# Performance work log

Measured on AMD Instinct MI355X. Metric: run time of the kernel, lower is better.

The kernel has to match this reference:

```python
import jax, jax.numpy as jnp
import numpy as np

D_MODEL = 1024
SEL_DIM = 64
CONFIGS = [(4, 32), (8, 64), (16, 128)]  # (heads, dim)
B, T = 2, 2048


def setup_inputs() -> dict:
    key = jax.random.key(0)
    ks = jax.random.split(key, 20)
    s = 0.02  # init scale for stability
    inp = {
        "x": jax.random.normal(ks[0], (B, T, D_MODEL), jnp.float32),
        "sel_w1": jax.random.normal(ks[1], (SEL_DIM, D_MODEL), jnp.float32) * s,
        "sel_b1": jnp.zeros((SEL_DIM,), jnp.float32),
        "sel_w2": jax.random.normal(ks[2], (SEL_DIM, SEL_DIM), jnp.float32) * s,
        "sel_b2": jnp.zeros((SEL_DIM,), jnp.float32),
        "sel_w3": jax.random.normal(ks[3], (len(CONFIGS), SEL_DIM), jnp.float32) * s,
        "sel_b3": jnp.zeros((len(CONFIGS),), jnp.float32),
    }
    for i, (h, d) in enumerate(CONFIGS):
        inp[f"qw{i}"] = jax.random.normal(ks[4 + 3 * i], (h * d, D_MODEL), jnp.float32) * s
        inp[f"kw{i}"] = jax.random.normal(ks[5 + 3 * i], (d, D_MODEL), jnp.float32) * s
        inp[f"ww{i}"] = jax.random.normal(ks[6 + 3 * i], (h, D_MODEL), jnp.float32) * s
    return inp


def _seq_features(x):
    # x: [b,t,d]
    b, t, d = x.shape
    seq_mean = jnp.mean(x, axis=1, keepdims=True)            # [b,1,d]
    seq_std = jnp.std(x, axis=1, keepdims=True, ddof=1)      # torch.std is unbiased
    pos = (jnp.arange(t, dtype=x.dtype) / t)[None, :, None]  # [1,t,1] broadcast to [b,t,d]
    return x + seq_mean + seq_std + pos * 0.1


def _forward(x, sel_w1, sel_b1, sel_w2, sel_b2, sel_w3, sel_b3,
             qw0, kw0, ww0, qw1, kw1, ww1, qw2, kw2, ww2):
    b, t, dm = x.shape
    feats = _seq_features(x)
    h1 = jax.nn.relu(feats @ sel_w1.T + sel_b1)
    h2 = jax.nn.relu(h1 @ sel_w2.T + sel_b2)
    config_probs = jax.nn.softmax(h2 @ sel_w3.T + sel_b3, axis=-1)  # [b,t,ncfg]

    per_cfg = [(qw0, kw0, ww0), (qw1, kw1, ww1), (qw2, kw2, ww2)]
    final = jnp.zeros((b, t, t), dtype=x.dtype)
    for i, ((heads, dim), (qw, kw, ww)) in enumerate(zip(CONFIGS, per_cfg)):
        q = (x @ qw.T).reshape(b, t, heads, dim)   # [b,t,h,d]
        k = x @ kw.T                               # [b,s,d]
        w = x @ ww.T                               # [b,t,h]
        dots = jnp.einsum('bthd,bsd->bths', q, k)  # [b,t,h,s]
        score = jnp.einsum('bths,bth->bts', jax.nn.relu(dots), w)  # relu*weight, sum heads
        final = final + config_probs[:, :, i:i + 1] * score
    return final


def reference(x, sel_w1, sel_b1, sel_w2, sel_b2, sel_w3, sel_b3,
              qw0, kw0, ww0, qw1, kw1, ww1, qw2, kw2, ww2):
    return _forward(x, sel_w1, sel_b1, sel_w2, sel_b2, sel_w3, sel_b3,
                    qw0, kw0, ww0, qw1, kw1, ww1, qw2, kw2, ww2)
```

## Files before the change

### kernel.cpp

```cpp
#include <hip/hip_runtime.h>
#include <hip/hip_fp16.h>
#include <cstdint>
#include <cstddef>
#include <math.h>

#define B_ 2
#define T_ 2048
#define D_ 1024
#define M_ (B_*T_)

#define QO0 0
#define KO0 128
#define WO0 160
#define QO1 168
#define KO1 680
#define WO1 744
#define QO2 752
#define KO2 2800
#define WO2 2928
#define SELO 2944
#define LDN 3072

typedef float f32x16 __attribute__((ext_vector_type(16)));
typedef short bf16x8 __attribute__((ext_vector_type(8)));
typedef unsigned short u16;

__device__ __forceinline__ u16 f2bf(float f) {
    unsigned int u = __float_as_uint(f);
    unsigned int r = (u + 0x7fffu + ((u >> 16) & 1u)) >> 16;
    return (u16)r;
}
__device__ __forceinline__ float bf2f(u16 b) {
    return __uint_as_float(((unsigned int)b) << 16);
}

__device__ __forceinline__ void gload16(const void* g, void* l) {
    __builtin_amdgcn_global_load_lds(
        (const __attribute__((address_space(1))) unsigned int*)g,
        (__attribute__((address_space(3))) unsigned int*)l,
        16, 0, 0);
}

__device__ __forceinline__ void stage_plane(const u16* src_base, int row_stride, int k0,
                                            int rg, int lane, u16* dst) {
    int rl  = lane >> 2;
    int row = rg * 16 + rl;
    int q   = (lane & 3) ^ (rl & 3) ^ ((rl >> 2) & 3);
    const u16* s = src_base + (size_t)row * row_stride + k0 + q * 8;
    gload16(s, dst + rg * 512);
}

__global__ void stats1(const float* __restrict__ x, float* __restrict__ part,
                       float* __restrict__ part2, u16* __restrict__ Xh) {
    int d  = blockIdx.x * 256 + threadIdx.x;
    int tc = blockIdx.y;
    int b  = blockIdx.z;
    size_t base = (size_t)b * T_ * D_ + (size_t)tc * 16 * D_ + d;
    float s = 0.f, s2 = 0.f;
#pragma unroll
    for (int t = 0; t < 16; ++t) {
        float v = x[base + (size_t)t * D_];
        s += v; s2 += v * v;
        Xh[base + (size_t)t * D_] = f2bf(v);
    }
    part [(b * 128 + tc) * D_ + d] = s;
    part2[(b * 128 + tc) * D_ + d] = s2;
}

__global__ void stats2(const float* __restrict__ part, const float* __restrict__ part2,
                       const float* __restrict__ w1,
                       float* __restrict__ msd, float* __restrict__ s1) {
    __shared__ float msL[1024];
    __shared__ float ps[64][17];
    __shared__ float pw[64][17];
    int b = blockIdx.x, tid = threadIdx.x;
    float s = 0.f, s2 = 0.f;
#pragma unroll 8
    for (int i = 0; i < 128; ++i) {
        s  += part [(b * 128 + i) * D_ + tid];
        s2 += part2[(b * 128 + i) * D_ + tid];
    }
    float mean = s / (float)T_;
    float var  = (s2 - (float)T_ * mean * mean) / (float)(T_ - 1);
    msL[tid] = mean + sqrtf(fmaxf(var, 0.f));
    __syncthreads();
    int j = tid >> 4, cc = tid & 15;
    float am = 0.f, aw = 0.f;
    const float* wr = w1 + (size_t)j * D_ + cc * 64;
    const float* mr = msL + cc * 64;
    for (int dd = 0; dd < 64; ++dd) { float w = wr[dd]; am += mr[dd] * w; aw += w; }
    ps[j][cc] = am; pw[j][cc] = aw;
    __syncthreads();
    if (tid < 64) {
        float sm = 0.f, sw = 0.f;
        for (int i = 0; i < 16; ++i) { sm += ps[tid][i]; sw += pw[tid][i]; }
        msd[b * 64 + tid] = sm;
        if (b == 0) s1[tid] = sw;
    }
}

__global__ void split_w(const float* __restrict__ qw0, const float* __restrict__ kw0,
                        const float* __restrict__ ww0, const float* __restrict__ qw1,
                        const float* __restrict__ kw1, const float* __restrict__ ww1,
                        const float* __restrict__ qw2, const float* __restrict__ kw2,
                        const float* __restrict__ ww2, const float* __restrict__ w1s,
                        u16* __restrict__ Wh) {
    int row = blockIdx.x;
    int col = threadIdx.x * 4;
    const float* src = nullptr;
    if      (row < 128)  src = qw0 + (size_t)row * D_;
    else if (row < 160)  src = kw0 + (size_t)(row - 128) * D_;
    else if (row < 164)  src = ww0 + (size_t)(row - 160) * D_;
    else if (row < 168)  src = nullptr;
    else if (row < 680)  src = qw1 + (size_t)(row - 168) * D_;
    else if (row < 744)  src = kw1 + (size_t)(row - 680) * D_;
    else if (row < 752)  src = ww1 + (size_t)(row - 744) * D_;
    else if (row < 2800) src = qw2 + (size_t)(row - 752) * D_;
    else if (row < 2928) src = kw2 + (size_t)(row - 2800) * D_;
    else if (row < 2944) src = ww2 + (size_t)(row - 2928) * D_;
    else if (row < 3008) src = w1s + (size_t)(row - 2944) * D_;
    float4 v = src ? *(const float4*)(src + col) : make_float4(0.f, 0.f, 0.f, 0.f);
    ushort4 h;
    h.x = f2bf(v.x); h.y = f2bf(v.y); h.z = f2bf(v.z); h.w = f2bf(v.w);
    *(ushort4*)&Wh[(size_t)row * D_ + col] = h;
}

__global__ __launch_bounds__(256, 3) void proj_gemm(
    const u16* __restrict__ Xh, const u16* __restrict__ Wh, u16* __restrict__ Ph) {
    __shared__ u16 As[8192], Bs[8192];
    int tid = threadIdx.x;
    int wave = tid >> 6, lane = tid & 63;
    int bm = blockIdx.x * 128, bn = blockIdx.y * 128;
    int wt = wave >> 1, wn = wave & 1;
    int fm = lane & 31, hv = lane >> 5;
    int tkey = (fm & 3) ^ ((fm >> 2) & 3);
    f32x16 acc[2][2];
#pragma unroll
    for (int i = 0; i < 2; ++i)
#pragma unroll
        for (int j = 0; j < 2; ++j)
#pragma unroll
            for (int r = 0; r < 16; ++r) acc[i][j][r] = 0.f;

    const u16* xh = Xh + (size_t)bm * D_;
    const u16* wh = Wh + (size_t)bn * D_;

    for (int kc = 0; kc < 16; ++kc) {
        int k0 = kc * 64;
#pragma unroll
        for (int i = 0; i < 8; ++i) {
            int j = wave * 8 + i;
            int mat = j >> 4;
            int pl  = (j >> 3) & 1;
            int rg  = j & 7;
            stage_plane(mat ? wh : xh, D_, k0 + pl * 32, rg, lane,
                        (mat ? Bs : As) + pl * 4096);
        }
        __syncthreads();
#pragma unroll
        for (int ks = 0; ks < 4; ++ks) {
            int pl = ks >> 1;
            int slot8 = (((ks & 1) * 2 + hv) ^ tkey) * 8;
            bf16x8 a_h[2], b_h[2];
#pragma unroll
            for (int t = 0; t < 2; ++t) {
                a_h[t] = *(const bf16x8*)&As[pl * 4096 + (wt * 64 + t * 32 + fm) * 32 + slot8];
                b_h[t] = *(const bf16x8*)&Bs[pl * 4096 + (wn * 64 + t * 32 + fm) * 32 + slot8];
            }
#pragma unroll
            for (int ti = 0; ti < 2; ++ti)
#pragma unroll
                for (int tj = 0; tj < 2; ++tj)
                    acc[ti][tj] = __builtin_amdgcn_mfma_f32_32x32x16_bf16(a_h[ti], b_h[tj], acc[ti][tj], 0, 0, 0);
        }
        __syncthreads();
    }
#pragma unroll
    for (int ti = 0; ti < 2; ++ti)
#pragma unroll
        for (int tj = 0; tj < 2; ++tj)
#pragma unroll
            for (int r = 0; r < 16; ++r) {
                int row = bm + wt * 64 + ti * 32 + (r & 3) + 8 * (r >> 2) + 4 * hv;
                int col = bn + wn * 64 + tj * 32 + fm;
                Ph[(size_t)row * LDN + col] = f2bf(acc[ti][tj][r]);
            }
}

__global__ void selector2(const u16* __restrict__ Ph,
                          const float* __restrict__ msd, const float* __restrict__ s1,
                          const float* __restrict__ b1, const float* __restrict__ w2,
                          const float* __restrict__ b2, const float* __restrict__ w3,
                          const float* __restrict__ b3, __half* __restrict__ WP) {
    __shared__ float h1s[4][64];
    __shared__ float h2s[4][64];
    __shared__ float lg[4][3];
    int tid = threadIdx.x;
    int slot = tid >> 6, j = tid & 63;
    int bt = blockIdx.x * 4 + slot;
    int b = bt >> 11, t = bt & 2047;
    size_t pidx = (size_t)bt * LDN + SELO + j;
    float v = bf2f(Ph[pidx])
            + msd[b * 64 + j] + 0.1f * ((float)t / (float)T_) * s1[j] + b1[j];
    h1s[slot][j] = fmaxf(v, 0.f);
    __syncthreads();
    float a2 = b2[j];
#pragma unroll 8
    for (int d = 0; d < 64; ++d) a2 = fmaf(h1s[slot][d], w2[j * 64 + d], a2);
    h2s[slot][j] = fmaxf(a2, 0.f);
    __syncthreads();
    if (j < 3) {
        float a3 = b3[j];
        for (int d = 0; d < 64; ++d) a3 = fmaf(h2s[slot][d], w3[j * 64 + d], a3);
        lg[slot][j] = a3;
    }
    __syncthreads();
    if (j < 28) {
        float m = fmaxf(lg[slot][0], fmaxf(lg[slot][1], lg[slot][2]));
        float e0 = expf(lg[slot][0] - m), e1 = expf(lg[slot][1] - m), e2 = expf(lg[slot][2] - m);
        float inv = 1.f / (e0 + e1 + e2);
        int wcol = (j < 4) ? (WO0 + j) : ((j < 12) ? (WO1 + j - 4) : (WO2 + j - 12));
        float p = ((j < 4) ? e0 : ((j < 12) ? e1 : e2)) * inv;
        float w = bf2f(Ph[(size_t)bt * LDN + wcol]);
        WP[(size_t)(b * 28 + j) * T_ + t] = __float2half(w * p);
    }
}

__device__ __forceinline__ int qcol_of(int c) {
    if (c < 2)  return QO0 + c * 64;
    if (c < 10) return QO1 + (c - 2) * 64;
    return QO2 + (c - 10) * 64;
}

__global__ __launch_bounds__(256, 2) void score_kernel(
    const u16* __restrict__ Ph, const __half* __restrict__ WP, float* __restrict__ out) {
    __shared__ u16 Qs[2][8192];
    __shared__ u16 Ks[4 * 4096];
    __shared__ __half wpL[3584];
    int tid = threadIdx.x;
    int wave = tid >> 6, lane = tid & 63;
    int wt = wave >> 1, wn = wave & 1;
    int fm = lane & 31, hv = lane >> 5;
    int tkey = (fm & 3) ^ ((fm >> 2) & 3);

    int n = blockIdx.z * 256 + blockIdx.y * 16 + blockIdx.x;
    int p = (n & 7) * 4 + (n >> 7);
    int xb = (n >> 3) & 15;
    int b = p >> 4, yb = p & 15;
    int t0 = yb * 128, s0 = xb * 128;

    const u16* Pq = Ph + (size_t)(b * T_ + t0) * LDN;
    const u16* Pk = Ph + (size_t)(b * T_ + s0) * LDN;

    auto stageQ = [&](int buf, int qcol) {
#pragma unroll
        for (int i = 0; i < 4; ++i) {
            int j = (wave << 2) + i;
            int pl = j >> 3, rg = j & 7;
            stage_plane(Pq, LDN, qcol + pl * 32, rg, lane, &Qs[buf][pl * 4096]);
        }
    };

#pragma unroll
    for (int i = 0; i < 6; ++i) {
        int j = i * 4 + wave;
        int pl = j >> 3, rg = j & 7;
        int col = (pl == 0) ? KO0 : ((pl == 1) ? KO1 : KO1 + 32);
        stage_plane(Pk, LDN, col, rg, lane, &Ks[pl * 4096]);
    }
#pragma unroll
    for (int i = 0; i < 2; ++i) {
        int j = i * 4 + wave;
        if (j < 7) {
            const __half* src = WP + (size_t)(b * 28 + j * 4 + (lane >> 4)) * T_ + t0 + (lane & 15) * 8;
            gload16(src, (u16*)wpL + j * 512);
        }
    }
    stageQ(0, QO0);

    f32x16 outacc[2][2], dots[2][2], Z16;
#pragma unroll
    for (int r = 0; r < 16; ++r) Z16[r] = 0.f;
#pragma unroll
    for (int i = 0; i < 2; ++i)
#pragma unroll
        for (int j = 0; j < 2; ++j)
#pragma unroll
            for (int r = 0; r < 16; ++r) { outacc[i][j][r] = 0.f; dots[i][j][r] = 0.f; }

    auto epi = [&](int g) {
#pragma unroll
        for (int ti = 0; ti < 2; ++ti) {
            int rowbase = wt * 64 + ti * 32 + 4 * hv;
#pragma unroll
            for (int rq = 0; rq < 4; ++rq) {
                const __half2* wp2 = (const __half2*)&wpL[g * 128 + rowbase + rq * 8];
                float2 f01 = __half22float2(wp2[0]);
                float2 f23 = __half22float2(wp2[1]);
                float wv[4] = {f01.x, f01.y, f23.x, f23.y};
#pragma unroll
                for (int tj = 0; tj < 2; ++tj)
#pragma unroll
                    for (int r2 = 0; r2 < 4; ++r2) {
                        int r = rq * 4 + r2;
                        outacc[ti][tj][r] += fmaxf(dots[ti][tj][r], 0.f) * wv[r2];
                    }
            }
        }
    };

    auto phase64 = [&](const u16* qb, int kpA, int kpB, bool z0, bool midBreak,
                       int gMid, bool hasEnd, int gEnd) {
#pragma unroll
        for (int ks = 0; ks < 4; ++ks) {
            int kp = (ks < 2) ? kpA : kpB;
            int slot8 = (((ks & 1) * 2 + hv) ^ tkey) * 8;
            bool zero = (ks == 0 && z0) || (ks == 2 && midBreak);
            bf16x8 kf[2], qf[2];
#pragma unroll
            for (int tj = 0; tj < 2; ++tj)
                kf[tj] = *(const bf16x8*)&Ks[kp * 4096 + (wn * 64 + tj * 32 + fm) * 32 + slot8];
#pragma unroll
            for (int ti = 0; ti < 2; ++ti)
                qf[ti] = *(const bf16x8*)&qb[(ks >> 1) * 4096 + (wt * 64 + ti * 32 + fm) * 32 + slot8];
#pragma unroll
            for (int ti = 0; ti < 2; ++ti)
#pragma unroll
                for (int tj = 0; tj < 2; ++tj)
                    dots[ti][tj] = __builtin_amdgcn_mfma_f32_32x32x16_bf16(
                        qf[ti], kf[tj], zero ? Z16 : dots[ti][tj], 0, 0, 0);
            if (ks == 1 && midBreak) epi(gMid);
            if (ks == 3 && hasEnd)   epi(gEnd);
        }
    };

#pragma unroll
    for (int c = 0; c < 2; ++c) {
        __syncthreads();
        stageQ((c + 1) & 1, qcol_of(c + 1));
        phase64(Qs[c & 1], 0, 0, true, true, 2 * c, true, 2 * c + 1);
    }
    for (int h = 0; h < 8; ++h) {
        int c = 2 + h;
        __syncthreads();
        stageQ((c + 1) & 1, qcol_of(c + 1));
        phase64(Qs[c & 1], 1, 2, true, false, -1, true, 4 + h);
        if (h == 7) {
            __syncthreads();
            for (int j = wave; j < 32; j += 4) {
                int pl = j >> 3, rg = j & 7;
                stage_plane(Pk, LDN, KO2 + pl * 32, rg, lane, &Ks[pl * 4096]);
            }
        }
    }
    for (int h = 0; h < 16; ++h) {
        int c = 10 + 2 * h;
        __syncthreads();
        stageQ((c + 1) & 1, qcol_of(c + 1));
        phase64(Qs[c & 1], 0, 1, true, false, -1, false, -1);
        __syncthreads();
        if (c + 1 < 41) stageQ(c & 1, qcol_of(c + 2));
        phase64(Qs[(c + 1) & 1], 2, 3, false, false, -1, true, 12 + h);
    }

#pragma unroll
    for (int ti = 0; ti < 2; ++ti)
#pragma unroll
        for (int tj = 0; tj < 2; ++tj)
#pragma unroll
            for (int r = 0; r < 16; ++r) {
                int trow = wt * 64 + ti * 32 + (r & 3) + 8 * (r >> 2) + 4 * hv;
                int scol = wn * 64 + tj * 32 + fm;
                out[(size_t)(b * T_ + t0 + trow) * T_ + (s0 + scol)] = outacc[ti][tj][r];
            }
}

extern "C" void kernel_launch(void* const* d_in, const int* in_sizes, int n_in,
                              void* d_out, int out_size, void* d_ws, size_t ws_size,
                              hipStream_t stream) {
    const float* x   = (const float*)d_in[0];
    const float* w1  = (const float*)d_in[1];
    const float* b1  = (const float*)d_in[2];
    const float* w2  = (const float*)d_in[3];
    const float* b2  = (const float*)d_in[4];
    const float* w3  = (const float*)d_in[5];
    const float* b3  = (const float*)d_in[6];
    const float* qw0 = (const float*)d_in[7];
    const float* kw0 = (const float*)d_in[8];
    const float* ww0 = (const float*)d_in[9];
    const float* qw1 = (const float*)d_in[10];
    const float* kw1 = (const float*)d_in[11];
    const float* ww1 = (const float*)d_in[12];
    const float* qw2 = (const float*)d_in[13];
    const float* kw2 = (const float*)d_in[14];
    const float* ww2 = (const float*)d_in[15];
    float* out = (float*)d_out;

    float* fb = (float*)d_ws;
    float* PA  = fb; fb += (size_t)B_ * 128 * D_;
    float* PA2 = fb; fb += (size_t)B_ * 128 * D_;
    float* MSD = fb; fb += 128;
    float* S1  = fb; fb += 64;
    __half* WP = (__half*)fb; fb += (size_t)B_ * 28 * T_ / 2;
    u16* ub = (u16*)fb;
    u16* Wh = ub; ub += (size_t)LDN * D_;
    u16* Xh = ub; ub += (size_t)M_ * D_;
    u16* Ph = ub; ub += (size_t)M_ * LDN;

    stats1<<<dim3(D_ / 256, 128, B_), 256, 0, stream>>>(x, PA, PA2, Xh);
    stats2<<<dim3(B_), 1024, 0, stream>>>(PA, PA2, w1, MSD, S1);
    split_w<<<dim3(LDN), 256, 0, stream>>>(qw0, kw0, ww0, qw1, kw1, ww1,
                                           qw2, kw2, ww2, w1, Wh);
    proj_gemm<<<dim3(M_ / 128, LDN / 128), 256, 0, stream>>>(Xh, Wh, Ph);
    selector2<<<dim3(M_ / 4), 256, 0, stream>>>(Ph, MSD, S1, b1, w2, b2, w3, b3, WP);
    score_kernel<<<dim3(T_ / 128, T_ / 128, B_), 256, 0, stream>>>(Ph, WP, out);
}
```

Baseline: 255.6 us.

## Software-pipeline LDS fragment loads and use split barriers in score kernel

The score kernel's phase loop becomes runPhase. It issues the next Q stage, waits with a partial vmcnt, and uses raw s_barrier with sched_barrier in place of __syncthreads. LDS fragment loads are double-buffered one k-step ahead, and MFMA blocks are wrapped in setprio to hide LDS latency behind matrix ops. Separately, stats1 now covers 64 rows per block instead of 16, which cuts the partial-sum buffers and the stats2 reduction by 4x. This adds register pressure and tighter hand-managed wait counts, which could be wrong if stageQ's load count does not match vmcnt(4).

Result: faster. 250.6 us (-2.0%).

```diff
diff --git a/kernel.cpp b/kernel.cpp
--- a/kernel.cpp
+++ b/kernel.cpp
@@ -55,16 +55,16 @@
     int d  = blockIdx.x * 256 + threadIdx.x;
     int tc = blockIdx.y;
     int b  = blockIdx.z;
-    size_t base = (size_t)b * T_ * D_ + (size_t)tc * 16 * D_ + d;
+    size_t base = (size_t)b * T_ * D_ + (size_t)tc * 64 * D_ + d;
     float s = 0.f, s2 = 0.f;
-#pragma unroll
-    for (int t = 0; t < 16; ++t) {
+#pragma unroll 8
+    for (int t = 0; t < 64; ++t) {
         float v = x[base + (size_t)t * D_];
         s += v; s2 += v * v;
         Xh[base + (size_t)t * D_] = f2bf(v);
     }
-    part [(b * 128 + tc) * D_ + d] = s;
-    part2[(b * 128 + tc) * D_ + d] = s2;
+    part [(b * 32 + tc) * D_ + d] = s;
+    part2[(b * 32 + tc) * D_ + d] = s2;
 }
 
 __global__ void stats2(const float* __restrict__ part, const float* __restrict__ part2,
@@ -76,9 +76,9 @@
     int b = blockIdx.x, tid = threadIdx.x;
     float s = 0.f, s2 = 0.f;
 #pragma unroll 8
-    for (int i = 0; i < 128; ++i) {
-        s  += part [(b * 128 + i) * D_ + tid];
-        s2 += part2[(b * 128 + i) * D_ + tid];
+    for (int i = 0; i < 32; ++i) {
+        s  += part [(b * 32 + i) * D_ + tid];
+        s2 += part2[(b * 32 + i) * D_ + tid];
     }
     float mean = s / (float)T_;
     float var  = (s2 - (float)T_ * mean * mean) / (float)(T_ - 1);
@@ -309,44 +309,56 @@
         }
     };
 
-    auto phase64 = [&](const u16* qb, int kpA, int kpB, bool z0, bool midBreak,
-                       int gMid, bool hasEnd, int gEnd) {
-#pragma unroll
-        for (int ks = 0; ks < 4; ++ks) {
+    auto runPhase = [&](int c, int kpA, int kpB, bool z0, bool midBreak,
+                        int gMid, bool hasEnd, int gEnd) {
+        if (c + 1 < 42) {
+            stageQ((c + 1) & 1, qcol_of(c + 1));
+            asm volatile("s_waitcnt vmcnt(4)" ::: "memory");
+        } else {
+            asm volatile("s_waitcnt vmcnt(0)" ::: "memory");
+        }
+        __builtin_amdgcn_s_barrier();
+        __builtin_amdgcn_sched_barrier(0);
+        const u16* qb = Qs[c & 1];
+
+        bf16x8 kf[2][2], qf[2][2];
+        auto loadks = [&](int ks, int sl) {
             int kp = (ks < 2) ? kpA : kpB;
             int slot8 = (((ks & 1) * 2 + hv) ^ tkey) * 8;
+#pragma unroll
+            for (int tj = 0; tj < 2; ++tj)
+                kf[sl][tj] = *(const bf16x8*)&Ks[kp * 4096 + (wn * 64 + tj * 32 + fm) * 32 + slot8];
+#pragma unroll
+            for (int ti = 0; ti < 2; ++ti)
+                qf[sl][ti] = *(const bf16x8*)&qb[(ks >> 1) * 4096 + (wt * 64 + ti * 32 + fm) * 32 + slot8];
+        };
+        loadks(0, 0);
+#pragma unroll
+        for (int ks = 0; ks < 4; ++ks) {
+            if (ks < 3) loadks(ks + 1, (ks + 1) & 1);
             bool zero = (ks == 0 && z0) || (ks == 2 && midBreak);
-            bf16x8 kf[2], qf[2];
-#pragma unroll
-            for (int tj = 0; tj < 2; ++tj)
-                kf[tj] = *(const bf16x8*)&Ks[kp * 4096 + (wn * 64 + tj * 32 + fm) * 32 + slot8];
-#pragma unroll
-            for (int ti = 0; ti < 2; ++ti)
-                qf[ti] = *(const bf16x8*)&qb[(ks >> 1) * 4096 + (wt * 64 + ti * 32 + fm) * 32 + slot8];
+            int sl = ks & 1;
+            __builtin_amdgcn_s_setprio(1);
 #pragma unroll
             for (int ti = 0; ti < 2; ++ti)
 #pragma unroll
                 for (int tj = 0; tj < 2; ++tj)
                     dots[ti][tj] = __builtin_amdgcn_mfma_f32_32x32x16_bf16(
-                        qf[ti], kf[tj], zero ? Z16 : dots[ti][tj], 0, 0, 0);
+                        qf[sl][ti], kf[sl][tj], zero ? Z16 : dots[ti][tj], 0, 0, 0);
+            __builtin_amdgcn_s_setprio(0);
             if (ks == 1 && midBreak) epi(gMid);
             if (ks == 3 && hasEnd)   epi(gEnd);
         }
+        __builtin_amdgcn_sched_barrier(0);
+        __builtin_amdgcn_s_barrier();
     };
 
 #pragma unroll
-    for (int c = 0; c < 2; ++c) {
-        __syncthreads();
-        stageQ((c + 1) & 1, qcol_of(c + 1));
-        phase64(Qs[c & 1], 0, 0, true, true, 2 * c, true, 2 * c + 1);
-    }
+    for (int c = 0; c < 2; ++c)
+        runPhase(c, 0, 0, true, true, 2 * c, true, 2 * c + 1);
     for (int h = 0; h < 8; ++h) {
-        int c = 2 + h;
-        __syncthreads();
-        stageQ((c + 1) & 1, qcol_of(c + 1));
-        phase64(Qs[c & 1], 1, 2, true, false, -1, true, 4 + h);
+        runPhase(2 + h, 1, 2, true, false, -1, true, 4 + h);
         if (h == 7) {
-            __syncthreads();
             for (int j = wave; j < 32; j += 4) {
                 int pl = j >> 3, rg = j & 7;
                 stage_plane(Pk, LDN, KO2 + pl * 32, rg, lane, &Ks[pl * 4096]);
@@ -354,13 +366,8 @@
         }
     }
     for (int h = 0; h < 16; ++h) {
-        int c = 10 + 2 * h;
-        __syncthreads();
-        stageQ((c + 1) & 1, qcol_of(c + 1));
-        phase64(Qs[c & 1], 0, 1, true, false, -1, false, -1);
-        __syncthreads();
-        if (c + 1 < 41) stageQ(c & 1, qcol_of(c + 2));
-        phase64(Qs[(c + 1) & 1], 2, 3, false, false, -1, true, 12 + h);
+        runPhase(10 + 2 * h, 0, 1, true, false, -1, false, -1);
+        runPhase(11 + 2 * h, 2, 3, false, false, -1, true, 12 + h);
     }
 
 #pragma unroll
@@ -397,8 +404,8 @@
     float* out = (float*)d_out;
 
     float* fb = (float*)d_ws;
-    float* PA  = fb; fb += (size_t)B_ * 128 * D_;
-    float* PA2 = fb; fb += (size_t)B_ * 128 * D_;
+    float* PA  = fb; fb += (size_t)B_ * 32 * D_;
+    float* PA2 = fb; fb += (size_t)B_ * 32 * D_;
     float* MSD = fb; fb += 128;
     float* S1  = fb; fb += 64;
     __half* WP = (__half*)fb; fb += (size_t)B_ * 28 * T_ / 2;
@@ -407,7 +414,7 @@
     u16* Xh = ub; ub += (size_t)M_ * D_;
     u16* Ph = ub; ub += (size_t)M_ * LDN;
 
-    stats1<<<dim3(D_ / 256, 128, B_), 256, 0, stream>>>(x, PA, PA2, Xh);
+    stats1<<<dim3(D_ / 256, 32, B_), 256, 0, stream>>>(x, PA, PA2, Xh);
     stats2<<<dim3(B_), 1024, 0, stream>>>(PA, PA2, w1, MSD, S1);
     split_w<<<dim3(LDN), 256, 0, stream>>>(qw0, kw0, ww0, qw1, kw1, ww1,
                                            qw2, kw2, ww2, w1, Wh);
```
